# Kernel optimization log

Measured on AMD Instinct MI355X. Metric: run time of the kernel, lower is better.

Reference implementation:

```python
import jax, jax.numpy as jnp
import numpy as np

K = 4096       # num_codebook_vectors
D = 256        # latent_dim
BETA = 0.25


def setup_inputs() -> dict:
    key = jax.random.key(0)
    k1, k2 = jax.random.split(key)
    z = jax.random.normal(k1, (16, D, 64, 64), dtype=jnp.float32)
    # nn.Embedding init: uniform(-1/K, 1/K)
    emb = jax.random.uniform(k2, (K, D), dtype=jnp.float32, minval=-1.0 / K, maxval=1.0 / K)
    return {"z": z, "emb": emb}


def reference(z, emb):
    B, C, H, W = z.shape
    zp = jnp.transpose(z, (0, 2, 3, 1))            # [B,H,W,C]
    zf = zp.reshape(-1, C)                          # [N,C]
    # squared L2 distances: ||z||^2 + ||e||^2 - 2 z.e
    d = (jnp.sum(zf * zf, axis=1, keepdims=True)
         + jnp.sum(emb * emb, axis=1)
         - 2.0 * jnp.matmul(zf, emb.T))             # [N,K]
    idx = jnp.argmin(d, axis=1)                     # [N]
    z_q = jnp.take(emb, idx, axis=0).reshape(zp.shape)  # [B,H,W,C]
    loss = (jnp.mean((jax.lax.stop_gradient(z_q) - zp) ** 2)
            + BETA * jnp.mean((z_q - jax.lax.stop_gradient(zp)) ** 2))
    # straight-through estimator
    z_q = zp + jax.lax.stop_gradient(z_q - zp)
    z_q = jnp.transpose(z_q, (0, 3, 1, 2))          # back to NCHW
    return z_q, idx, loss
```

## Files before the change

kernel.cpp:

```cpp
#include <hip/hip_runtime.h>
#include <math.h>

#define KCODES 4096
#define DIM    256
#define HW     4096
#define NPIX   65536
#define NQ     16777216
#define EPSW   3.0e-4f

typedef _Float16 f16x8 __attribute__((ext_vector_type(8)));
typedef float    f32x4 __attribute__((ext_vector_type(4)));

#define SWZ(x) ((x) ^ ((((x) >> 6) & 7) << 4))

static __device__ __forceinline__ void gld16(const void* g, void* l) {
    __builtin_amdgcn_global_load_lds(
        (const __attribute__((address_space(1))) void*)g,
        (__attribute__((address_space(3))) void*)l, 16, 0, 0);
}

#define INS4(V, I, dd, kk) do { \
  if ((dd) < V[3]) { \
    if ((dd) < V[1]) { \
      V[3]=V[2]; I[3]=I[2]; V[2]=V[1]; I[2]=I[1]; \
      if ((dd) < V[0]) { V[1]=V[0]; I[1]=I[0]; V[0]=(dd); I[0]=(kk); } \
      else             { V[1]=(dd); I[1]=(kk); } \
    } else { \
      if ((dd) < V[2]) { V[3]=V[2]; I[3]=I[2]; V[2]=(dd); I[2]=(kk); } \
      else             { V[3]=(dd); I[3]=(kk); } \
    } } } while(0)

#define INS8(V, I, dd, kk) do { \
  if ((dd) < V[7]) { \
    if ((dd) < V[3]) { \
      V[7]=V[6];I[7]=I[6];V[6]=V[5];I[6]=I[5];V[5]=V[4];I[5]=I[4];V[4]=V[3];I[4]=I[3]; \
      if ((dd) < V[1]) { \
        V[3]=V[2];I[3]=I[2];V[2]=V[1];I[2]=I[1]; \
        if ((dd) < V[0]) { V[1]=V[0];I[1]=I[0];V[0]=(dd);I[0]=(kk); } \
        else             { V[1]=(dd);I[1]=(kk); } \
      } else { \
        if ((dd) < V[2]) { V[3]=V[2];I[3]=I[2];V[2]=(dd);I[2]=(kk); } \
        else             { V[3]=(dd);I[3]=(kk); } \
      } \
    } else { \
      if ((dd) < V[5]) { \
        V[7]=V[6];I[7]=I[6];V[6]=V[5];I[6]=I[5]; \
        if ((dd) < V[4]) { V[5]=V[4];I[5]=I[4];V[4]=(dd);I[4]=(kk); } \
        else             { V[5]=(dd);I[5]=(kk); } \
      } else { \
        if ((dd) < V[6]) { V[7]=V[6];I[7]=I[6];V[6]=(dd);I[6]=(kk); } \
        else             { V[7]=(dd);I[7]=(kk); } \
      } \
    } } } while(0)

__global__ __launch_bounds__(256) void ee_np_kernel(const float* __restrict__ emb,
                                                    float* __restrict__ ee) {
#pragma clang fp contract(off)
    const int k = blockIdx.x * 256 + threadIdx.x;
    const float* a = emb + (size_t)k * DIM;
    float res[2];
    #pragma unroll
    for (int h = 0; h < 2; ++h) {
        const float* b = a + h * 128;
        float r[8];
        #pragma unroll
        for (int j = 0; j < 8; ++j) { const float x = b[j]; r[j] = x * x; }
        for (int i = 8; i < 128; i += 8) {
            #pragma unroll
            for (int j = 0; j < 8; ++j) { const float x = b[i + j]; r[j] += x * x; }
        }
        res[h] = ((r[0] + r[1]) + (r[2] + r[3])) + ((r[4] + r[5]) + (r[6] + r[7]));
    }
    ee[k] = res[0] + res[1];
}

__global__ __launch_bounds__(256) void zz_np_kernel(const float* __restrict__ z,
                                                    float* __restrict__ zz) {
#pragma clang fp contract(off)
    const int n  = blockIdx.x * 256 + threadIdx.x;
    const int b  = n >> 12;
    const int hw = n & (HW - 1);
    const float* base = z + (size_t)b * DIM * HW + hw;
    float res[2];
    #pragma unroll
    for (int h = 0; h < 2; ++h) {
        const float* p = base + (size_t)(h * 128) * HW;
        float r[8];
        #pragma unroll
        for (int j = 0; j < 8; ++j) { const float x = p[(size_t)j * HW]; r[j] = x * x; }
        for (int i = 8; i < 128; i += 8) {
            #pragma unroll
            for (int j = 0; j < 8; ++j) { const float x = p[(size_t)(i + j) * HW]; r[j] += x * x; }
        }
        res[h] = ((r[0] + r[1]) + (r[2] + r[3])) + ((r[4] + r[5]) + (r[6] + r[7]));
    }
    zz[n] = res[0] + res[1];
}

__device__ float np_dist(const float* __restrict__ z, const float* __restrict__ emb,
                         const float* __restrict__ zz, const float* __restrict__ ee,
                         int n, int k) {
    const int b = n >> 12, hw = n & (HW - 1);
    const float* zp = z + (size_t)b * DIM * HW + hw;
    const float* ep = emb + (size_t)k * DIM;
    float m = 0.0f;
    for (int i = 0; i < DIM; ++i) m = fmaf(zp[(size_t)i * HW], ep[i], m);
    const float t = zz[n] + ee[k];
    return t - 2.0f * m;
}

__global__ __launch_bounds__(256) void cvt_emb_kernel(const float* __restrict__ emb,
                                                      ushort* __restrict__ eh) {
    const int t = threadIdx.x;
    const int k = blockIdx.x * 4 + (t >> 6);
    const int seg = t & 63;
    const float4 v = *reinterpret_cast<const float4*>(emb + (size_t)k * DIM + seg * 4);
    union H4 { _Float16 h[4]; short4 s; } uh;
    const float vv[4] = {v.x, v.y, v.z, v.w};
    #pragma unroll
    for (int j = 0; j < 4; ++j) uh.h[j] = (_Float16)(vv[j] * 4096.0f);
    const int s = seg >> 3;
    const int y  = (k & 127) * 64 + (seg & 7) * 8;
    const int ys = y ^ ((k & 7) << 4);
    const size_t addr = (size_t)(k >> 7) * 32768 + s * 4096 + (ys >> 1);
    *reinterpret_cast<short4*>(eh + addr) = uh.s;
}

__global__ __launch_bounds__(256) void cvt_z_kernel(const float* __restrict__ z,
                                                    ushort* __restrict__ zh) {
    __shared__ float ls[64][65];
    const int t = threadIdx.x;
    const int bid = blockIdx.x;
    const int b = bid >> 8, cc = (bid >> 6) & 3, hh = bid & 63;
    const int col = t & 63, r0 = t >> 6;
    #pragma unroll
    for (int i = 0; i < 16; ++i) {
        const int r = i * 4 + r0;
        ls[r][col] = z[((size_t)(b * DIM + cc * 64 + r)) * HW + hh * 64 + col];
    }
    __syncthreads();
    const int pxl = t >> 2, cseg = t & 3;
    const int px = b * HW + hh * 64 + pxl;
    const int sg = cc * 2 + (cseg >> 1);
    union H8 { _Float16 h[8]; int4 v; } ha, hb;
    #pragma unroll
    for (int j = 0; j < 16; ++j) {
        const float val = ls[cseg * 16 + j][pxl];
        if (j < 8) ha.h[j] = (_Float16)val;
        else       hb.h[j - 8] = (_Float16)val;
    }
    const size_t chunk = (size_t)(px >> 7) * 32768 + sg * 4096;
    const int y1  = (px & 127) * 64 + (cseg & 1) * 32;
    const int msk = (px & 7) << 4;
    *reinterpret_cast<int4*>(zh + chunk + ((y1 ^ msk) >> 1))        = ha.v;
    *reinterpret_cast<int4*>(zh + chunk + (((y1 + 16) ^ msk) >> 1)) = hb.v;
}

__global__ __launch_bounds__(256, 3) void gemm_kernel(const ushort* __restrict__ eh,
                                                      const ushort* __restrict__ zh,
                                                      const float* __restrict__ ee,
                                                      const float* __restrict__ zz,
                                                      float* __restrict__ top8v,
                                                      int* __restrict__ top8i,
                                                      float* __restrict__ m3f) {
    __shared__ __align__(16) char et[2][16384];

    const int t = threadIdx.x;
    const int lane = t & 63, w = t >> 6, wr = w >> 1, wc = w & 1;
    const int l15 = lane & 15, l4 = lane >> 4;
    const int bid = blockIdx.x;
    const int px0 = bid * 64;
    const int lo = t * 16;
    const int wb = w * 1024;
    const char* ehB = (const char*)eh;

    f16x8 zr[2][8];
    {
        const size_t chunk = (size_t)(bid >> 1) * 32768;
        #pragma unroll
        for (int ni = 0; ni < 2; ++ni) {
            const int lr = (bid & 1) * 64 + wc * 32 + ni * 16 + l15;
            const int ro = SWZ(lr * 64 + l4 * 16) >> 1;
            #pragma unroll
            for (int s = 0; s < 8; ++s)
                zr[ni][s] = *reinterpret_cast<const f16x8*>(zh + chunk + s * 4096 + ro);
        }
    }
    float zzr[2];
    #pragma unroll
    for (int ni = 0; ni < 2; ++ni) zzr[ni] = zz[px0 + wc * 32 + ni * 16 + l15];

    int aoff[4];
    #pragma unroll
    for (int mi = 0; mi < 4; ++mi)
        aoff[mi] = SWZ((wr * 64 + mi * 16 + l15) * 64 + l4 * 16);

    #pragma unroll
    for (int r = 0; r < 4; ++r)
        gld16(ehB + r * 4096 + lo, et[0] + r * 4096 + wb);
    __syncthreads();

    float Tv[2][4]; int Ti[2][4];
    #pragma unroll
    for (int ni = 0; ni < 2; ++ni)
        #pragma unroll
        for (int j = 0; j < 4; ++j) { Tv[ni][j] = 3.0e38f; Ti[ni][j] = 0; }

    for (int p = 0; p < 32; ++p) {
        float eer[4][4];
        #pragma unroll
        for (int mi = 0; mi < 4; ++mi)
            #pragma unroll
            for (int r = 0; r < 4; ++r)
                eer[mi][r] = ee[p * 128 + wr * 64 + mi * 16 + l4 * 4 + r];

        f32x4 acc[4][2];
        #pragma unroll
        for (int mi = 0; mi < 4; ++mi)
            #pragma unroll
            for (int ni = 0; ni < 2; ++ni)
                acc[mi][ni] = (f32x4){0.0f, 0.0f, 0.0f, 0.0f};

        #pragma unroll
        for (int st = 0; st < 4; ++st) {
            const int cur = st & 1;
            if (st < 3 || p < 31) {
                const size_t nb = ((size_t)(p * 4 + st) + 1) * 16384;
                #pragma unroll
                for (int r = 0; r < 4; ++r)
                    gld16(ehB + nb + r * 4096 + lo, et[cur ^ 1] + r * 4096 + wb);
            }
            #pragma unroll
            for (int sp = 0; sp < 2; ++sp) {
                const int sg = st * 2 + sp;
                f16x8 aH[4];
                #pragma unroll
                for (int mi = 0; mi < 4; ++mi)
                    aH[mi] = *reinterpret_cast<const f16x8*>(et[cur] + sp * 8192 + aoff[mi]);
                #pragma unroll
                for (int mi = 0; mi < 4; ++mi)
                    #pragma unroll
                    for (int ni = 0; ni < 2; ++ni)
                        acc[mi][ni] = __builtin_amdgcn_mfma_f32_16x16x32_f16(aH[mi], zr[ni][sg], acc[mi][ni], 0, 0, 0);
            }
            __syncthreads();
        }
        #pragma unroll
        for (int ni = 0; ni < 2; ++ni) {
            const float zzc = zzr[ni];
            #pragma unroll
            for (int mi = 0; mi < 4; ++mi) {
                #pragma unroll
                for (int r = 0; r < 4; ++r) {
                    const float tt = zzc + eer[mi][r];
                    const float d = fmaf(acc[mi][ni][r], -4.8828125e-4f, tt);
                    const int k = p * 128 + wr * 64 + mi * 16 + l4 * 4 + r;
                    INS4(Tv[ni], Ti[ni], d, k);
                }
            }
        }
    }

    float (*mv)[64][8]  = reinterpret_cast<float (*)[64][8]>(&et[0][0]);
    int   (*mi_)[64][8] = reinterpret_cast<int (*)[64][8]>(&et[0][8192]);
    float (*m3s)[64]    = reinterpret_cast<float (*)[64]>(&et[1][0]);

    #pragma unroll
    for (int ni = 0; ni < 2; ++ni) {
        float fv[8]; int fi[8];
        #pragma unroll
        for (int j = 0; j < 4; ++j) { fv[j] = Tv[ni][j]; fi[j] = Ti[ni][j]; }
        #pragma unroll
        for (int j = 4; j < 8; ++j) { fv[j] = 3.0e38f; fi[j] = 0; }
        float m3 = Tv[ni][3];
        #pragma unroll
        for (int m = 16; m <= 32; m <<= 1) {
            float ov[8]; int oi[8];
            #pragma unroll
            for (int j = 0; j < 8; ++j) {
                ov[j] = __shfl_xor(fv[j], m, 64);
                oi[j] = __shfl_xor(fi[j], m, 64);
            }
            const float om = __shfl_xor(m3, m, 64);
            #pragma unroll
            for (int j = 0; j < 8; ++j) INS8(fv, fi, ov[j], oi[j]);
            m3 = fminf(m3, om);
        }
        if (lane < 16) {
            const int c = wc * 32 + ni * 16 + lane;
            #pragma unroll
            for (int j = 0; j < 8; ++j) { mv[wr][c][j] = fv[j]; mi_[wr][c][j] = fi[j]; }
            m3s[wr][c] = m3;
        }
    }
    __syncthreads();
    if (t < 64) {
        float fv[8]; int fi[8];
        #pragma unroll
        for (int j = 0; j < 8; ++j) { fv[j] = mv[0][t][j]; fi[j] = mi_[0][t][j]; }
        #pragma unroll
        for (int j = 0; j < 8; ++j) INS8(fv, fi, mv[1][t][j], mi_[1][t][j]);
        const float m3 = fminf(m3s[0][t], m3s[1][t]);
        const int px = px0 + t;
        *reinterpret_cast<float4*>(top8v + (size_t)px * 8)     = make_float4(fv[0], fv[1], fv[2], fv[3]);
        *reinterpret_cast<float4*>(top8v + (size_t)px * 8 + 4) = make_float4(fv[4], fv[5], fv[6], fv[7]);
        *reinterpret_cast<int4*>(top8i + (size_t)px * 8)       = make_int4(fi[0], fi[1], fi[2], fi[3]);
        *reinterpret_cast<int4*>(top8i + (size_t)px * 8 + 4)   = make_int4(fi[4], fi[5], fi[6], fi[7]);
        m3f[px] = m3;
    }
}

__global__ __launch_bounds__(256) void resolve_kernel(const float* __restrict__ z,
                                                      const float* __restrict__ emb,
                                                      const float* __restrict__ zz,
                                                      const float* __restrict__ ee,
                                                      const float* __restrict__ top8v,
                                                      const int* __restrict__ top8i,
                                                      const float* __restrict__ m3f,
                                                      int* __restrict__ idxf,
                                                      int* __restrict__ cnt,
                                                      int* __restrict__ rlist) {
    const int n = blockIdx.x * 256 + threadIdx.x;
    float v[8]; int id[8];
    {
        const float4 v0 = *reinterpret_cast<const float4*>(top8v + (size_t)n * 8);
        const float4 v1 = *reinterpret_cast<const float4*>(top8v + (size_t)n * 8 + 4);
        const int4   i0 = *reinterpret_cast<const int4*>(top8i + (size_t)n * 8);
        const int4   i1 = *reinterpret_cast<const int4*>(top8i + (size_t)n * 8 + 4);
        v[0]=v0.x; v[1]=v0.y; v[2]=v0.z; v[3]=v0.w; v[4]=v1.x; v[5]=v1.y; v[6]=v1.z; v[7]=v1.w;
        id[0]=i0.x; id[1]=i0.y; id[2]=i0.z; id[3]=i0.w; id[4]=i1.x; id[5]=i1.y; id[6]=i1.z; id[7]=i1.w;
    }
    const float lim = v[0] + EPSW;
    if (v[7] <= lim || m3f[n] <= lim) {
        idxf[n] = id[0];
        const int pos = atomicAdd(cnt, 1);
        rlist[pos] = n;
        return;
    }
    if (v[1] > lim) { idxf[n] = id[0]; return; }
    int ck[8]; int nc = 0;
    for (int j = 0; j < 8; ++j) if (v[j] <= lim) ck[nc++] = id[j];
    for (int a = 0; a < nc - 1; ++a)
        for (int b2 = a + 1; b2 < nc; ++b2)
            if (ck[b2] < ck[a]) { int tmp = ck[a]; ck[a] = ck[b2]; ck[b2] = tmp; }
    float best = 0.0f; int bk = -1;
    for (int a = 0; a < nc; ++a) {
        const float d = np_dist(z, emb, zz, ee, n, ck[a]);
        if (bk < 0 || d < best) { best = d; bk = ck[a]; }
    }
    idxf[n] = bk;
}

__global__ __launch_bounds__(256) void rescan_kernel(const float* __restrict__ z,
                                                     const float* __restrict__ emb,
                                                     const float* __restrict__ zz,
                                                     const float* __restrict__ ee,
                                                     const int* __restrict__ cnt,
                                                     const int* __restrict__ rlist,
                                                     int* __restrict__ idxf) {
#pragma clang fp contract(off)
    __shared__ float ls[DIM];
    __shared__ float wv[4];
    __shared__ int   wk[4];
    const int t = threadIdx.x;
    const int lane = t & 63, w = t >> 6;
    const int count = *cnt;
    for (int e = blockIdx.x; e < count; e += gridDim.x) {
        const int n = rlist[e];
        const int b = n >> 12, hw = n & (HW - 1);
        __syncthreads();
        ls[t] = z[((size_t)(b * DIM + t)) * HW + hw];
        __syncthreads();
        const float zzn = zz[n];
        float bestd = 3.0e38f; int besti = 0x7fffffff;
        for (int j = 0; j < 16; ++j) {
            const int k = t + j * 256;
            const float* ep = emb + (size_t)k * DIM;
            float m = 0.0f;
            for (int i = 0; i < DIM; ++i) m = fmaf(ls[i], ep[i], m);
            const float d = (zzn + ee[k]) - 2.0f * m;
            if (d < bestd || (d == bestd && k < besti)) { bestd = d; besti = k; }
        }
        #pragma unroll
        for (int off = 32; off >= 1; off >>= 1) {
            const float od = __shfl_down(bestd, off, 64);
            const int   ok = __shfl_down(besti, off, 64);
            if (od < bestd || (od == bestd && ok < besti)) { bestd = od; besti = ok; }
        }
        if (lane == 0) { wv[w] = bestd; wk[w] = besti; }
        __syncthreads();
        if (t == 0) {
            float bd = wv[0]; int bi = wk[0];
            #pragma unroll
            for (int q = 1; q < 4; ++q)
                if (wv[q] < bd || (wv[q] == bd && wk[q] < bi)) { bd = wv[q]; bi = wk[q]; }
            idxf[n] = bi;
        }
    }
}

__global__ __launch_bounds__(256) void gather_kernel(const float* __restrict__ z,
                                                     const float* __restrict__ emb,
                                                     const int* __restrict__ idxf,
                                                     float* __restrict__ out,
                                                     float* __restrict__ part) {
    __shared__ int   idx_s[32];
    __shared__ float wred[4];
    const int tid = threadIdx.x;
    const int tx = tid & 31, ty = tid >> 5;
    const int m0 = blockIdx.x * 32;
    const int bimg = m0 >> 12, hw0 = m0 & (HW - 1);
    if (tid < 32) {
        const int ii = idxf[m0 + tid];
        idx_s[tid] = ii;
        out[NQ + m0 + tid] = (float)ii;
    }
    __syncthreads();
    float lsum = 0.0f;
    const size_t ebase = (size_t)idx_s[tx] * DIM;
    for (int it = 0; it < DIM / 8; ++it) {
        const int c = it * 8 + ty;
        const float e = emb[ebase + c];
        const size_t zoff = ((size_t)(bimg * DIM + c)) * HW + hw0 + tx;
        out[zoff] = e;
        const float diff = e - z[zoff];
        lsum += diff * diff;
    }
    #pragma unroll
    for (int off = 32; off >= 1; off >>= 1) lsum += __shfl_down(lsum, off, 64);
    if ((tid & 63) == 0) wred[tid >> 6] = lsum;
    __syncthreads();
    if (tid == 0) part[blockIdx.x] = wred[0] + wred[1] + wred[2] + wred[3];
}

__global__ __launch_bounds__(256) void loss_kernel(const float* __restrict__ part,
                                                   int nblk, float* __restrict__ out) {
    __shared__ float wred[4];
    const int tid = threadIdx.x;
    float s = 0.0f;
    for (int i = tid; i < nblk; i += 256) s += part[i];
    #pragma unroll
    for (int off = 32; off >= 1; off >>= 1) s += __shfl_down(s, off, 64);
    if ((tid & 63) == 0) wred[tid >> 6] = s;
    __syncthreads();
    if (tid == 0) {
        const float total = wred[0] + wred[1] + wred[2] + wred[3];
        out[NQ + NPIX] = 1.25f * total / 16777216.0f;
    }
}

#define MP 32
#define KC 128
#define DC 32
__global__ __launch_bounds__(256) void safe_dist_kernel(const float* __restrict__ z,
                                                        const float* __restrict__ emb,
                                                        const float* __restrict__ ee,
                                                        const float* __restrict__ zz,
                                                        float* __restrict__ out,
                                                        float* __restrict__ part) {
    __shared__ float zs[MP][DIM + 4];
    __shared__ float est[DC][KC + 4];
    __shared__ float ee_s[KC];
    __shared__ float zz_s[MP];
    __shared__ float red_v[MP][33];
    __shared__ int   red_i[MP][33];
    __shared__ int   idx_s[MP];
    __shared__ float wred[4];

    const int tid = threadIdx.x;
    const int tx = tid & 31, ty = tid >> 5;
    const int m0 = blockIdx.x * MP;
    const int bimg = m0 >> 12, hw0 = m0 & (HW - 1);

    for (int c = ty; c < DIM; c += 8)
        zs[tx][c] = z[((size_t)(bimg * DIM + c)) * HW + hw0 + tx];
    if (tid < MP) zz_s[tid] = zz[m0 + tid];

    float minv[4]; int mini[4];
    #pragma unroll
    for (int p = 0; p < 4; ++p) { minv[p] = 3.0e38f; mini[p] = 0; }
    const int rl = tid >> 3, cl = tid & 7;

    for (int kc = 0; kc < KCODES / KC; ++kc) {
        float acc[4][4];
        #pragma unroll
        for (int p = 0; p < 4; ++p)
            #pragma unroll
            for (int q = 0; q < 4; ++q) acc[p][q] = 0.0f;
        for (int dc = 0; dc < DIM / DC; ++dc) {
            __syncthreads();
            if (dc == 0 && tid < KC) ee_s[tid] = ee[kc * KC + tid];
            #pragma unroll
            for (int it = 0; it < 4; ++it) {
                const int kl = it * 32 + rl;
                const float4 v = *reinterpret_cast<const float4*>(
                    emb + (size_t)(kc * KC + kl) * DIM + dc * DC + cl * 4);
                est[cl * 4 + 0][kl] = v.x;
                est[cl * 4 + 1][kl] = v.y;
                est[cl * 4 + 2][kl] = v.z;
                est[cl * 4 + 3][kl] = v.w;
            }
            __syncthreads();
            #pragma unroll
            for (int g = 0; g < DC / 4; ++g) {
                float4 zr[4];
                #pragma unroll
                for (int p = 0; p < 4; ++p)
                    zr[p] = *reinterpret_cast<const float4*>(&zs[ty * 4 + p][dc * DC + g * 4]);
                float4 er[4];
                #pragma unroll
                for (int j = 0; j < 4; ++j)
                    er[j] = *reinterpret_cast<const float4*>(&est[g * 4 + j][tx * 4]);
                #pragma unroll
                for (int p = 0; p < 4; ++p) {
                    acc[p][0] = fmaf(zr[p].x, er[0].x, acc[p][0]);
                    acc[p][0] = fmaf(zr[p].y, er[1].x, acc[p][0]);
                    acc[p][0] = fmaf(zr[p].z, er[2].x, acc[p][0]);
                    acc[p][0] = fmaf(zr[p].w, er[3].x, acc[p][0]);
                    acc[p][1] = fmaf(zr[p].x, er[0].y, acc[p][1]);
                    acc[p][1] = fmaf(zr[p].y, er[1].y, acc[p][1]);
                    acc[p][1] = fmaf(zr[p].z, er[2].y, acc[p][1]);
                    acc[p][1] = fmaf(zr[p].w, er[3].y, acc[p][1]);
                    acc[p][2] = fmaf(zr[p].x, er[0].z, acc[p][2]);
                    acc[p][2] = fmaf(zr[p].y, er[1].z, acc[p][2]);
                    acc[p][2] = fmaf(zr[p].z, er[2].z, acc[p][2]);
                    acc[p][2] = fmaf(zr[p].w, er[3].z, acc[p][2]);
                    acc[p][3] = fmaf(zr[p].x, er[0].w, acc[p][3]);
                    acc[p][3] = fmaf(zr[p].y, er[1].w, acc[p][3]);
                    acc[p][3] = fmaf(zr[p].z, er[2].w, acc[p][3]);
                    acc[p][3] = fmaf(zr[p].w, er[3].w, acc[p][3]);
                }
            }
        }
        #pragma unroll
        for (int q = 0; q < 4; ++q) {
            const int kg = kc * KC + tx * 4 + q;
            const float en = ee_s[tx * 4 + q];
            #pragma unroll
            for (int p = 0; p < 4; ++p) {
                const float t = zz_s[ty * 4 + p] + en;
                const float d = t - 2.0f * acc[p][q];
                if (d < minv[p]) { minv[p] = d; mini[p] = kg; }
            }
        }
    }
    #pragma unroll
    for (int p = 0; p < 4; ++p) {
        red_v[ty * 4 + p][tx] = minv[p];
        red_i[ty * 4 + p][tx] = mini[p];
    }
    __syncthreads();
    if (tid < MP) {
        float bvv = red_v[tid][0]; int bii = red_i[tid][0];
        for (int q = 1; q < 32; ++q) {
            const float vq = red_v[tid][q]; const int iq = red_i[tid][q];
            if (vq < bvv || (vq == bvv && iq < bii)) { bvv = vq; bii = iq; }
        }
        idx_s[tid] = bii;
        out[NQ + m0 + tid] = (float)bii;
    }
    __syncthreads();
    float lsum = 0.0f;
    const size_t ebase = (size_t)idx_s[tx] * DIM;
    for (int it = 0; it < DIM / 8; ++it) {
        const int c = it * 8 + ty;
        const float e = emb[ebase + c];
        out[((size_t)(bimg * DIM + c)) * HW + hw0 + tx] = e;
        const float diff = e - zs[tx][c];
        lsum += diff * diff;
    }
    #pragma unroll
    for (int off = 32; off >= 1; off >>= 1) lsum += __shfl_down(lsum, off, 64);
    if ((tid & 63) == 0) wred[tid >> 6] = lsum;
    __syncthreads();
    if (tid == 0) part[blockIdx.x] = wred[0] + wred[1] + wred[2] + wred[3];
}

extern "C" void kernel_launch(void* const* d_in, const int* in_sizes, int n_in,
                              void* d_out, int out_size, void* d_ws, size_t ws_size,
                              hipStream_t stream) {
    const float* z   = (const float*)d_in[0];
    const float* emb = (const float*)d_in[1];
    float* out = (float*)d_out;
    char*  ws  = (char*)d_ws;

    float* zz   = (float*)(ws + 0);
    float* ee   = (float*)(ws + 262144);
    float* part = (float*)(ws + 278528);
    int*   cnt  = (int*)  (ws + 286720);
    int*   rlst = (int*)  (ws + 290816);
    int*   idxf = (int*)  (ws + 552960);
    float* t8v  = (float*)(ws + 1048576);
    int*   t8i  = (int*)  (ws + 3145728);
    ushort* eh  = (ushort*)(ws + 5242880);
    ushort* zh  = (ushort*)(ws + 7340032);
    float* m3f  = (float*)(ws + 40894464);
    const size_t REQ = 74448896;

    ee_np_kernel<<<KCODES / 256, 256, 0, stream>>>(emb, ee);
    zz_np_kernel<<<NPIX / 256, 256, 0, stream>>>(z, zz);

    if (ws_size >= REQ) {
        hipMemsetAsync(cnt, 0, 4, stream);
        cvt_emb_kernel<<<KCODES / 4, 256, 0, stream>>>(emb, eh);
        cvt_z_kernel<<<4096, 256, 0, stream>>>(z, zh);
        gemm_kernel<<<NPIX / 64, 256, 0, stream>>>(eh, zh, ee, zz, t8v, t8i, m3f);
        resolve_kernel<<<NPIX / 256, 256, 0, stream>>>(z, emb, zz, ee, t8v, t8i, m3f, idxf, cnt, rlst);
        rescan_kernel<<<2048, 256, 0, stream>>>(z, emb, zz, ee, cnt, rlst, idxf);
        gather_kernel<<<NPIX / 32, 256, 0, stream>>>(z, emb, idxf, out, part);
        loss_kernel<<<1, 256, 0, stream>>>(part, NPIX / 32, out);
    } else {
        safe_dist_kernel<<<NPIX / MP, 256, 0, stream>>>(z, emb, ee, zz, out, part);
        loss_kernel<<<1, 256, 0, stream>>>(part, NPIX / MP, out);
    }
}
```

Measured before the change: 543.9 us.

## Triple-buffer codebook tiles in LDS with one barrier per stage and LDS-staged norms

Replaces the double-buffered codebook staging with a three-buffer rotating pipeline. Each stage prefetches two tiles ahead and uses a single barrier guarded by a partial vmcnt wait instead of a trailing __syncthreads. All codebook norms (ee) are now loaded into LDS once up front, so the per-block global loads of norms go away, and the p/st loops are flattened into one loop. LDS use rises to 64KB, so launch bounds drop from 3 to 2 blocks per CU, which lowers occupancy in exchange for deeper latency hiding.

Result: slower. 753.1 us (+38.5%).

```diff
diff --git a/kernel.cpp b/kernel.cpp
--- a/kernel.cpp
+++ b/kernel.cpp
@@ -156,14 +156,14 @@
     *reinterpret_cast<int4*>(zh + chunk + (((y1 + 16) ^ msk) >> 1)) = hb.v;
 }
 
-__global__ __launch_bounds__(256, 3) void gemm_kernel(const ushort* __restrict__ eh,
+__global__ __launch_bounds__(256, 2) void gemm_kernel(const ushort* __restrict__ eh,
                                                       const ushort* __restrict__ zh,
                                                       const float* __restrict__ ee,
                                                       const float* __restrict__ zz,
                                                       float* __restrict__ top8v,
                                                       int* __restrict__ top8i,
                                                       float* __restrict__ m3f) {
-    __shared__ __align__(16) char et[2][16384];
+    __shared__ __align__(16) char lds[65536];
 
     const int t = threadIdx.x;
     const int lane = t & 63, w = t >> 6, wr = w >> 1, wc = w & 1;
@@ -173,6 +173,7 @@
     const int lo = t * 16;
     const int wb = w * 1024;
     const char* ehB = (const char*)eh;
+    char* const eel = lds + 49152;
 
     f16x8 zr[2][8];
     {
@@ -197,8 +198,13 @@
 
     #pragma unroll
     for (int r = 0; r < 4; ++r)
-        gld16(ehB + r * 4096 + lo, et[0] + r * 4096 + wb);
-    __syncthreads();
+        gld16((const char*)ee + r * 4096 + lo, eel + r * 4096 + wb);
+    #pragma unroll
+    for (int r = 0; r < 4; ++r)
+        gld16(ehB + r * 4096 + lo, lds + r * 4096 + wb);
+    #pragma unroll
+    for (int r = 0; r < 4; ++r)
+        gld16(ehB + 16384 + r * 4096 + lo, lds + 16384 + r * 4096 + wb);
 
     float Tv[2][4]; int Ti[2][4];
     #pragma unroll
@@ -206,64 +212,72 @@
         #pragma unroll
         for (int j = 0; j < 4; ++j) { Tv[ni][j] = 3.0e38f; Ti[ni][j] = 0; }
 
-    for (int p = 0; p < 32; ++p) {
-        float eer[4][4];
-        #pragma unroll
-        for (int mi = 0; mi < 4; ++mi)
+    f32x4 acc[4][2];
+    char* B0 = lds;
+    char* B1 = lds + 16384;
+    char* B2 = lds + 32768;
+
+    for (int ph = 0; ph < 128; ++ph) {
+        const int p = ph >> 2, st = ph & 3;
+        asm volatile("s_waitcnt vmcnt(4)" ::: "memory");
+        __builtin_amdgcn_sched_barrier(0);
+        __builtin_amdgcn_s_barrier();
+        {
+            const size_t src = (size_t)((ph + 2) & 127) * 16384;
             #pragma unroll
             for (int r = 0; r < 4; ++r)
-                eer[mi][r] = ee[p * 128 + wr * 64 + mi * 16 + l4 * 4 + r];
-
-        f32x4 acc[4][2];
-        #pragma unroll
-        for (int mi = 0; mi < 4; ++mi)
-            #pragma unroll
-            for (int ni = 0; ni < 2; ++ni)
-                acc[mi][ni] = (f32x4){0.0f, 0.0f, 0.0f, 0.0f};
-
-        #pragma unroll
-        for (int st = 0; st < 4; ++st) {
-            const int cur = st & 1;
-            if (st < 3 || p < 31) {
-                const size_t nb = ((size_t)(p * 4 + st) + 1) * 16384;
+                gld16(ehB + src + r * 4096 + lo, B2 + r * 4096 + wb);
+        }
+        if (st == 0) {
+            #pragma unroll
+            for (int mi = 0; mi < 4; ++mi)
                 #pragma unroll
-                for (int r = 0; r < 4; ++r)
-                    gld16(ehB + nb + r * 4096 + lo, et[cur ^ 1] + r * 4096 + wb);
-            }
-            #pragma unroll
-            for (int sp = 0; sp < 2; ++sp) {
-                const int sg = st * 2 + sp;
-                f16x8 aH[4];
+                for (int ni = 0; ni < 2; ++ni)
+                    acc[mi][ni] = (f32x4){0.0f, 0.0f, 0.0f, 0.0f};
+        }
+        #pragma unroll
+        for (int sp = 0; sp < 2; ++sp) {
+            const int sg = st * 2 + sp;
+            f16x8 aH[4];
+            #pragma unroll
+            for (int mi = 0; mi < 4; ++mi)
+                aH[mi] = *reinterpret_cast<const f16x8*>(B0 + sp * 8192 + aoff[mi]);
+            #pragma unroll
+            for (int mi = 0; mi < 4; ++mi)
                 #pragma unroll
-                for (int mi = 0; mi < 4; ++mi)
-                    aH[mi] = *reinterpret_cast<const f16x8*>(et[cur] + sp * 8192 + aoff[mi]);
+                for (int ni = 0; ni < 2; ++ni)
+                    acc[mi][ni] = __builtin_amdgcn_mfma_f32_16x16x32_f16(aH[mi], zr[ni][sg], acc[mi][ni], 0, 0, 0);
+        }
+        if (st == 3) {
+            float eer[4][4];
+            #pragma unroll
+            for (int mi = 0; mi < 4; ++mi)
+                *reinterpret_cast<float4*>(&eer[mi][0]) =
+                    *reinterpret_cast<const float4*>(eel + (size_t)(p * 128 + wr * 64 + mi * 16 + l4 * 4) * 4);
+            #pragma unroll
+            for (int ni = 0; ni < 2; ++ni) {
+                const float zzc = zzr[ni];
                 #pragma unroll
-                for (int mi = 0; mi < 4; ++mi)
+                for (int mi = 0; mi < 4; ++mi) {
                     #pragma unroll
-                    for (int ni = 0; ni < 2; ++ni)
-                        acc[mi][ni] = __builtin_amdgcn_mfma_f32_16x16x32_f16(aH[mi], zr[ni][sg], acc[mi][ni], 0, 0, 0);
-            }
-            __syncthreads();
-        }
-        #pragma unroll
-        for (int ni = 0; ni < 2; ++ni) {
-            const float zzc = zzr[ni];
-            #pragma unroll
-            for (int mi = 0; mi < 4; ++mi) {
-                #pragma unroll
-                for (int r = 0; r < 4; ++r) {
-                    const float tt = zzc + eer[mi][r];
-                    const float d = fmaf(acc[mi][ni][r], -4.8828125e-4f, tt);
-                    const int k = p * 128 + wr * 64 + mi * 16 + l4 * 4 + r;
-                    INS4(Tv[ni], Ti[ni], d, k);
+                    for (int r = 0; r < 4; ++r) {
+                        const float tt = zzc + eer[mi][r];
+                        const float d = fmaf(acc[mi][ni][r], -4.8828125e-4f, tt);
+                        const int k = p * 128 + wr * 64 + mi * 16 + l4 * 4 + r;
+                        INS4(Tv[ni], Ti[ni], d, k);
+                    }
                 }
             }
         }
-    }
-
-    float (*mv)[64][8]  = reinterpret_cast<float (*)[64][8]>(&et[0][0]);
-    int   (*mi_)[64][8] = reinterpret_cast<int (*)[64][8]>(&et[0][8192]);
-    float (*m3s)[64]    = reinterpret_cast<float (*)[64]>(&et[1][0]);
+        char* tmp = B0; B0 = B1; B1 = B2; B2 = tmp;
+    }
+
+    asm volatile("s_waitcnt vmcnt(0)" ::: "memory");
+    __syncthreads();
+
+    float (*mv)[64][8]  = reinterpret_cast<float (*)[64][8]>(&lds[0]);
+    int   (*mi_)[64][8] = reinterpret_cast<int (*)[64][8]>(&lds[8192]);
+    float (*m3s)[64]    = reinterpret_cast<float (*)[64]>(&lds[16384]);
 
     #pragma unroll
     for (int ni = 0; ni < 2; ++ni) {
```

## Fuse per-pixel squared norm into z conversion and stage gathered codes in LDS

Applied to the files above, without the earlier changes.

The z-to-fp16 conversion kernel now loads all 256 channels of a 64-pixel row into shared memory and also computes each pixel's squared norm, which removes the separate zz kernel and its second full read of z on the fast path. The gather kernel first copies the 32 selected codebook rows into shared memory with coalesced reads, then reads them transposed, instead of issuing strided global loads per channel. In exchange, the conversion kernel uses about 66KB of LDS per block, which limits occupancy. The norm summation is written with contraction turned off and a fixed order, presumably to match the numerics of the original norm kernel.

New measurement: 520.3 us. -4.3%, faster.

```diff
diff --git a/kernel.cpp b/kernel.cpp
--- a/kernel.cpp
+++ b/kernel.cpp
@@ -127,33 +127,57 @@
 }
 
 __global__ __launch_bounds__(256) void cvt_z_kernel(const float* __restrict__ z,
-                                                    ushort* __restrict__ zh) {
-    __shared__ float ls[64][65];
+                                                    ushort* __restrict__ zh,
+                                                    float* __restrict__ zz) {
+#pragma clang fp contract(off)
+    __shared__ float ls[256][65];
     const int t = threadIdx.x;
     const int bid = blockIdx.x;
-    const int b = bid >> 8, cc = (bid >> 6) & 3, hh = bid & 63;
+    const int b = bid >> 6, hh = bid & 63;
     const int col = t & 63, r0 = t >> 6;
     #pragma unroll
-    for (int i = 0; i < 16; ++i) {
-        const int r = i * 4 + r0;
-        ls[r][col] = z[((size_t)(b * DIM + cc * 64 + r)) * HW + hh * 64 + col];
-    }
-    __syncthreads();
+    for (int i = 0; i < 64; ++i) {
+        const int c = i * 4 + r0;
+        ls[c][col] = z[((size_t)(b * DIM + c)) * HW + hh * 64 + col];
+    }
+    __syncthreads();
+
+    if (t < 64) {
+        float res[2];
+        #pragma unroll
+        for (int h = 0; h < 2; ++h) {
+            const int base = h * 128;
+            float r[8];
+            #pragma unroll
+            for (int j = 0; j < 8; ++j) { const float x = ls[base + j][t]; r[j] = x * x; }
+            for (int i = 8; i < 128; i += 8) {
+                #pragma unroll
+                for (int j = 0; j < 8; ++j) { const float x = ls[base + i + j][t]; r[j] += x * x; }
+            }
+            res[h] = ((r[0] + r[1]) + (r[2] + r[3])) + ((r[4] + r[5]) + (r[6] + r[7]));
+        }
+        zz[b * HW + hh * 64 + t] = res[0] + res[1];
+    }
+
     const int pxl = t >> 2, cseg = t & 3;
     const int px = b * HW + hh * 64 + pxl;
-    const int sg = cc * 2 + (cseg >> 1);
-    union H8 { _Float16 h[8]; int4 v; } ha, hb;
-    #pragma unroll
-    for (int j = 0; j < 16; ++j) {
-        const float val = ls[cseg * 16 + j][pxl];
-        if (j < 8) ha.h[j] = (_Float16)val;
-        else       hb.h[j - 8] = (_Float16)val;
-    }
-    const size_t chunk = (size_t)(px >> 7) * 32768 + sg * 4096;
-    const int y1  = (px & 127) * 64 + (cseg & 1) * 32;
+    const size_t chunkb = (size_t)(px >> 7) * 32768;
     const int msk = (px & 7) << 4;
-    *reinterpret_cast<int4*>(zh + chunk + ((y1 ^ msk) >> 1))        = ha.v;
-    *reinterpret_cast<int4*>(zh + chunk + (((y1 + 16) ^ msk) >> 1)) = hb.v;
+    #pragma unroll
+    for (int g = 0; g < 4; ++g) {
+        const int cb = cseg * 64 + g * 16;
+        union H8 { _Float16 h[8]; int4 v; } ha, hb;
+        #pragma unroll
+        for (int j = 0; j < 16; ++j) {
+            const float val = ls[cb + j][pxl];
+            if (j < 8) ha.h[j] = (_Float16)val;
+            else       hb.h[j - 8] = (_Float16)val;
+        }
+        const int sg = cb >> 5;
+        const int y1 = (px & 127) * 64 + ((cb >> 4) & 1) * 32;
+        *reinterpret_cast<int4*>(zh + chunkb + sg * 4096 + ((y1 ^ msk) >> 1))        = ha.v;
+        *reinterpret_cast<int4*>(zh + chunkb + sg * 4096 + (((y1 + 16) ^ msk) >> 1)) = hb.v;
+    }
 }
 
 __global__ __launch_bounds__(256, 3) void gemm_kernel(const ushort* __restrict__ eh,
@@ -405,6 +429,7 @@
                                                      float* __restrict__ out,
                                                      float* __restrict__ part) {
     __shared__ int   idx_s[32];
+    __shared__ float es[32][257];
     __shared__ float wred[4];
     const int tid = threadIdx.x;
     const int tx = tid & 31, ty = tid >> 5;
@@ -416,11 +441,13 @@
         out[NQ + m0 + tid] = (float)ii;
     }
     __syncthreads();
+    for (int r = 0; r < 32; ++r)
+        es[r][tid] = emb[(size_t)idx_s[r] * DIM + tid];
+    __syncthreads();
     float lsum = 0.0f;
-    const size_t ebase = (size_t)idx_s[tx] * DIM;
     for (int it = 0; it < DIM / 8; ++it) {
         const int c = it * 8 + ty;
-        const float e = emb[ebase + c];
+        const float e = es[tx][c];
         const size_t zoff = ((size_t)(bimg * DIM + c)) * HW + hw0 + tx;
         out[zoff] = e;
         const float diff = e - z[zoff];
@@ -598,18 +625,18 @@
     const size_t REQ = 74448896;
 
     ee_np_kernel<<<KCODES / 256, 256, 0, stream>>>(emb, ee);
-    zz_np_kernel<<<NPIX / 256, 256, 0, stream>>>(z, zz);
 
     if (ws_size >= REQ) {
         hipMemsetAsync(cnt, 0, 4, stream);
         cvt_emb_kernel<<<KCODES / 4, 256, 0, stream>>>(emb, eh);
-        cvt_z_kernel<<<4096, 256, 0, stream>>>(z, zh);
+        cvt_z_kernel<<<1024, 256, 0, stream>>>(z, zh, zz);
         gemm_kernel<<<NPIX / 64, 256, 0, stream>>>(eh, zh, ee, zz, t8v, t8i, m3f);
         resolve_kernel<<<NPIX / 256, 256, 0, stream>>>(z, emb, zz, ee, t8v, t8i, m3f, idxf, cnt, rlst);
         rescan_kernel<<<2048, 256, 0, stream>>>(z, emb, zz, ee, cnt, rlst, idxf);
         gather_kernel<<<NPIX / 32, 256, 0, stream>>>(z, emb, idxf, out, part);
         loss_kernel<<<1, 256, 0, stream>>>(part, NPIX / 32, out);
     } else {
+        zz_np_kernel<<<NPIX / 256, 256, 0, stream>>>(z, zz);
         safe_dist_kernel<<<NPIX / MP, 256, 0, stream>>>(z, emb, ee, zz, out, part);
         loss_kernel<<<1, 256, 0, stream>>>(part, NPIX / MP, out);
     }
```
